# Kernel tuning notes

Hardware: AMD Instinct MI355X
Metric: run time of the kernel (lower is better)

## Reference

```python
import jax, jax.numpy as jnp
import numpy as np

# Module config (init_kwargs)
CIN, COUT, KH, KW = 256, 256, 3, 3
STRIDE, PADDING = 1, 1
T = 64                 # psum chunk size along the reduction (K) axis
NBITS = 8              # saturating accumulator bits (signed)
QMAX = (1 << (NBITS - 1)) - 1   # 127
QMIN = QMAX - (1 << NBITS) + 1  # -128


def setup_inputs() -> dict:
    key = jax.random.key(0)
    k1, k2 = jax.random.split(key)
    x = jax.random.normal(k1, (8, CIN, 56, 56), dtype=jnp.float32)
    # nn.Parameter(torch.rand((N,1)) * 0.001)
    weights = jax.random.uniform(k2, (CIN * COUT * KH * KW, 1), dtype=jnp.float32) * 0.001
    return {"x": x, "weights": weights}


def reference(x, weights):
    B, _, H, W = x.shape
    OH = (H - KH + 2 * PADDING) // STRIDE + 1
    OW = (W - KW + 2 * PADDING) // STRIDE + 1

    w = weights.reshape(COUT, CIN, KH, KW)
    # per-output-channel scaling factor, detached
    scale = jax.lax.stop_gradient(jnp.mean(jnp.abs(w), axis=(1, 2, 3), keepdims=True))
    # binarize with STE: sign(w).detach() - clamp(w).detach() + clamp(w)
    wc = jnp.clip(w, -1.0, 1.0)
    wb = jax.lax.stop_gradient(jnp.sign(w) - wc) + wc

    # unfold (im2col); channel varies slowest -> matches torch.nn.functional.unfold
    patches = jax.lax.conv_general_dilated_patches(
        x, (KH, KW), (STRIDE, STRIDE), [(PADDING, PADDING), (PADDING, PADDING)]
    )  # [B, CIN*KH*KW, OH*OW... (spatial)]
    K = CIN * KH * KW
    L = OH * OW
    A = patches.reshape(B, K, L).transpose(0, 2, 1)  # [B, L, K]
    X = wb.reshape(COUT, K).T                        # [K, COUT]

    pad = (-K) % T
    if pad:
        A = jnp.pad(A, ((0, 0), (0, 0), (0, pad)))
        X = jnp.pad(X, ((0, pad), (0, 0)))
    nT = (K + pad) // T

    A4 = A.reshape(B, L, nT, T)        # chunked reduction axis
    X3 = X.reshape(nT, T, COUT)
    # per-chunk partial sums (satmm_cuda.forward_psum)
    psum = jnp.einsum('blnt,ntc->nblc', A4, X3)  # [nT, B, L, COUT]

    # saturating sequential accumulation: reduce(lambda a,b: clip(a+b, QMIN, QMAX))
    def step(carry, p):
        return jnp.clip(carry + p, QMIN, QMAX), None
    y_flat, _ = jax.lax.scan(step, psum[0], psum[1:])  # [B, L, COUT]

    y = y_flat.transpose(0, 2, 1).reshape(B, COUT, OH, OW)
    y = y * scale.reshape(1, -1, 1, 1)
    # psum returned in the original [B, L, COUT, nT] layout
    return y, psum.transpose(1, 2, 3, 0)
```

## Files before the change

kernel.cpp:

```cpp
#include <hip/hip_runtime.h>
#include <hip/hip_bf16.h>

#define CIN 256
#define COUT 256
#define HW 56
#define BATCH 8
#define L_SPATIAL 3136
#define K_TOTAL 2304
#define NT 36
#define NH 18
#define ROWF (COUT * NT)
#define KSTRIDE 2312
#define BUF_BYTES (16 * KSTRIDE * 2)
#define CARRY_OFF (2 * BUF_BYTES)
#define LDS_BYTES (CARRY_OFF + 8192)
#define MT_TOTAL 1568
#define TILES_PER_IMG 196
#define NWG 256
#define QMAXF 127.0f
#define QMINF -128.0f

typedef short bf16x8 __attribute__((ext_vector_type(8)));
typedef float f32x4 __attribute__((ext_vector_type(4)));
typedef float f32x2 __attribute__((ext_vector_type(2)));

__device__ __forceinline__ void nt_store4(float* p, f32x4 v) {
  __builtin_nontemporal_store(v, reinterpret_cast<f32x4*>(p));
}

__device__ __forceinline__ void lgkm_barrier() {
  __builtin_amdgcn_sched_barrier(0);
  asm volatile("s_waitcnt lgkmcnt(0)" ::: "memory");
  __builtin_amdgcn_s_barrier();
  asm volatile("" ::: "memory");
  __builtin_amdgcn_sched_barrier(0);
}

__global__ __launch_bounds__(256) void prep_kernel(
    const float* __restrict__ w, unsigned short* __restrict__ bsign,
    float* __restrict__ scale) {
  const int c = blockIdx.x;
  const int t = threadIdx.x;
  const float* row = w + (size_t)c * K_TOTAL;
  unsigned short* out = bsign + (size_t)c * K_TOTAL;
  float acc = 0.0f;
#pragma unroll
  for (int j = 0; j < 9; ++j) {
    const int k = t + 256 * j;
    const float v = row[k];
    acc += __builtin_fabsf(v);
    out[k] = (v > 0.0f) ? (unsigned short)0x3F80
           : ((v < 0.0f) ? (unsigned short)0xBF80 : (unsigned short)0);
  }
#pragma unroll
  for (int o = 32; o > 0; o >>= 1) acc += __shfl_down(acc, o, 64);
  __shared__ float red[4];
  if ((t & 63) == 0) red[t >> 6] = acc;
  __syncthreads();
  if (t == 0) scale[c] = (red[0] + red[1] + red[2] + red[3]) * (1.0f / 2304.0f);
}

__device__ __forceinline__ void build_atile(
    const float* __restrict__ xb, unsigned short* __restrict__ Atile,
    int tid, int l0) {
  const int ml = tid & 15;
  const int grp = tid >> 4;
  const int l = l0 + ml;
  const int oh = l / HW;
  const int ow = l - oh * HW;
  unsigned short* arow = Atile + ml * KSTRIDE;
  for (int r = grp; r < 768; r += 64) {
    const int ci = r / 3;
    const int kh = r - ci * 3;
    const int hh = oh + kh - 1;
    const bool hv = ((unsigned)hh < (unsigned)HW);
    const float* xr = xb + (ci * HW + hh) * HW;
    const int kb = ci * 9 + kh * 3;
#pragma unroll
    for (int kw = 0; kw < 3; ++kw) {
      const int wv = ow + kw - 1;
      float v = 0.0f;
      if (hv && ((unsigned)wv < (unsigned)HW)) v = xr[wv];
      __hip_bfloat16 bv = __float2bfloat16(v);
      arow[kb + kw] = *reinterpret_cast<unsigned short*>(&bv);
    }
  }
}

template <int H>
__device__ __forceinline__ void compute18(
    const unsigned short* __restrict__ aptr,
    const unsigned short* __restrict__ bptr,
    f32x4* __restrict__ ps, f32x4& sacc) {
  const f32x4 zero = {0.0f, 0.0f, 0.0f, 0.0f};
  const unsigned short* ap = aptr + H * NH * 64;
  const unsigned short* bp = bptr + H * NH * 64;
  bf16x8 b0[3], b1[3];
  b0[0] = *reinterpret_cast<const bf16x8*>(bp);
  b1[0] = *reinterpret_cast<const bf16x8*>(bp + 32);
  b0[1] = *reinterpret_cast<const bf16x8*>(bp + 64);
  b1[1] = *reinterpret_cast<const bf16x8*>(bp + 96);
#pragma unroll
  for (int j = 0; j < NH; ++j) {
    if (j + 2 < NH) {
      b0[(j + 2) % 3] = *reinterpret_cast<const bf16x8*>(bp + (j + 2) * 64);
      b1[(j + 2) % 3] = *reinterpret_cast<const bf16x8*>(bp + (j + 2) * 64 + 32);
    }
    bf16x8 a0 = *reinterpret_cast<const bf16x8*>(ap + j * 64);
    bf16x8 a1 = *reinterpret_cast<const bf16x8*>(ap + j * 64 + 32);
    f32x4 acc = __builtin_amdgcn_mfma_f32_16x16x32_bf16(a0, b0[j % 3], zero, 0, 0, 0);
    acc = __builtin_amdgcn_mfma_f32_16x16x32_bf16(a1, b1[j % 3], acc, 0, 0, 0);
    ps[j] = acc;
    if (H == 0) {
      if (j == 0) {
        sacc = acc;
      } else {
#pragma unroll
        for (int e = 0; e < 4; ++e)
          sacc[e] = __builtin_amdgcn_fmed3f(sacc[e] + acc[e], QMINF, QMAXF);
      }
    }
  }
}

__global__ __launch_bounds__(1024, 4) void satconv_kernel(
    const float* __restrict__ x, const unsigned short* __restrict__ bsign,
    const float* __restrict__ scale, float* __restrict__ y_out,
    float* __restrict__ psum_out) {
  extern __shared__ char smem[];
  float* carryb = (float*)(smem + CARRY_OFF);

  const int tid = threadIdx.x;
  const int w = blockIdx.x;
  const int b_img = w & 7;
  const float* xb = x + (size_t)b_img * (CIN * L_SPATIAL);

  const int lane = tid & 63;
  const int cl = lane & 15;
  const int q = lane >> 4;
  const int wave = tid >> 6;
  const int cs = wave >> 1;
  const int h = wave & 1;

  const float sc_s0 = scale[cs * 16 + cl];
  const float sc_s1 = scale[128 + cs * 16 + cl];

  int rel_it[9];
  {
#pragma unroll
    for (int it = 0; it < 9; ++it) {
      const int f = it * 256 + lane * 4;
      const int qq = f / 576;
      const int rem = f - qq * 576;
      const int ci = rem / 36;
      const int n0 = rem - ci * 36;
      rel_it[it] = ((qq << 2) * COUT + ci) * NT + n0;
    }
  }

  int p = 0;
  int t = w;
  build_atile(xb, (unsigned short*)smem, tid, (t >> 3) << 4);
  __syncthreads();

  while (t < MT_TOTAL) {
    const int l0 = (t >> 3) << 4;
    const int m0 = (b_img * TILES_PER_IMG + (t >> 3)) << 4;
    const int mbase = m0 * ROWF;
    unsigned short* Atile = (unsigned short*)(smem + p * BUF_BYTES);
    float* stage = (float*)(smem + (p ^ 1) * BUF_BYTES);
    float* reg = stage + cs * 2304;
    const unsigned short* aptr = Atile + cl * KSTRIDE + q * 8;

    for (int s = 0; s < 2; ++s) {
      const int csub0 = (s << 7) + (cs << 4);
      const int c = csub0 + cl;
      const unsigned short* bptr = bsign + (size_t)c * K_TOTAL + q * 8;

      f32x4 ps[NH];
      f32x4 sacc = {0.0f, 0.0f, 0.0f, 0.0f};
      if (h == 0) compute18<0>(aptr, bptr, ps, sacc);
      else        compute18<1>(aptr, bptr, ps, sacc);

      if (h == 0)
        *reinterpret_cast<f32x4*>(carryb + cs * 256 + lane * 4) = sacc;
      lgkm_barrier();
      if (h == 1) {
        f32x4 cin = *reinterpret_cast<const f32x4*>(carryb + cs * 256 + lane * 4);
#pragma unroll
        for (int j = 0; j < NH; ++j) {
#pragma unroll
          for (int e = 0; e < 4; ++e)
            cin[e] = __builtin_amdgcn_fmed3f(cin[e] + ps[j][e], QMINF, QMAXF);
        }
        const float sc = (s == 0) ? sc_s0 : sc_s1;
        f32x4 yv;
#pragma unroll
        for (int e = 0; e < 4; ++e) yv[e] = cin[e] * sc;
        nt_store4(y_out + ((size_t)b_img * COUT + c) * L_SPATIAL + l0 + (q << 2), yv);
      }

      const int soff = csub0 * NT;
#pragma unroll
      for (int rg = 0; rg < 4; ++rg) {
        {
          float* wr = reg + q * 576 + cl * 36 + h * NH;
          if (h == 0) {
            f32x4 v;
#pragma unroll
            for (int g = 0; g < 4; ++g) {
              v[0] = ps[4 * g + 0][rg]; v[1] = ps[4 * g + 1][rg];
              v[2] = ps[4 * g + 2][rg]; v[3] = ps[4 * g + 3][rg];
              *reinterpret_cast<f32x4*>(wr + 4 * g) = v;
            }
            f32x2 tl = {ps[16][rg], ps[17][rg]};
            *reinterpret_cast<f32x2*>(wr + 16) = tl;
          } else {
            f32x2 tl = {ps[0][rg], ps[1][rg]};
            *reinterpret_cast<f32x2*>(wr) = tl;
            f32x4 v;
#pragma unroll
            for (int g = 0; g < 4; ++g) {
              v[0] = ps[4 * g + 2][rg]; v[1] = ps[4 * g + 3][rg];
              v[2] = ps[4 * g + 4][rg]; v[3] = ps[4 * g + 5][rg];
              *reinterpret_cast<f32x4*>(wr + 2 + 4 * g) = v;
            }
          }
        }
        lgkm_barrier();
        {
          const int rgoff = rg * ROWF + soff;
          const int it0 = (h == 0) ? 0 : 5;
          const int it1 = (h == 0) ? 5 : 9;
          for (int it = it0; it < it1; ++it) {
            f32x4 v = *reinterpret_cast<const f32x4*>(reg + it * 256 + lane * 4);
            nt_store4(psum_out + (size_t)(mbase + rel_it[it] + rgoff), v);
          }
        }
        lgkm_barrier();
      }
    }

    const int tn = t + NWG;
    if (tn < MT_TOTAL)
      build_atile(xb, (unsigned short*)(smem + (p ^ 1) * BUF_BYTES), tid,
                  (tn >> 3) << 4);
    lgkm_barrier();
    p ^= 1;
    t = tn;
  }
}

extern "C" void kernel_launch(void* const* d_in, const int* in_sizes, int n_in,
                              void* d_out, int out_size, void* d_ws, size_t ws_size,
                              hipStream_t stream) {
  const float* x = (const float*)d_in[0];
  const float* w = (const float*)d_in[1];
  float* y = (float*)d_out;
  float* psum = y + (size_t)BATCH * COUT * L_SPATIAL;
  unsigned short* bsign = (unsigned short*)d_ws;
  float* scale = (float*)((char*)d_ws + (size_t)COUT * K_TOTAL * 2);

  prep_kernel<<<COUT, 256, 0, stream>>>(w, bsign, scale);

  hipFuncSetAttribute(reinterpret_cast<const void*>(satconv_kernel),
                      hipFuncAttributeMaxDynamicSharedMemorySize, LDS_BYTES);
  satconv_kernel<<<NWG, 1024, LDS_BYTES, stream>>>(
      x, bsign, scale, y, psum);
}
```

Baseline: 1.229 ms.

## Warp-specialize producer and drainer waves to overlap MFMA compute with psum stores

```diff
diff --git a/kernel.cpp b/kernel.cpp
--- a/kernel.cpp
+++ b/kernel.cpp
@@ -8,12 +8,15 @@
 #define L_SPATIAL 3136
 #define K_TOTAL 2304
 #define NT 36
-#define NH 18
+#define NTH 12
 #define ROWF (COUT * NT)
 #define KSTRIDE 2312
-#define BUF_BYTES (16 * KSTRIDE * 2)
-#define CARRY_OFF (2 * BUF_BYTES)
-#define LDS_BYTES (CARRY_OFF + 8192)
+#define ATILE_BYTES (16 * KSTRIDE * 2)
+#define SLOT0_OFF ATILE_BYTES
+#define SLOT1_OFF (ATILE_BYTES + 36864)
+#define CARRY_OFF (ATILE_BYTES + 73728)
+#define YSTAGE_OFF (CARRY_OFF + 4096)
+#define LDS_BYTES (YSTAGE_OFF + 4096)
 #define MT_TOTAL 1568
 #define TILES_PER_IMG 196
 #define NWG 256
@@ -22,7 +25,6 @@
 
 typedef short bf16x8 __attribute__((ext_vector_type(8)));
 typedef float f32x4 __attribute__((ext_vector_type(4)));
-typedef float f32x2 __attribute__((ext_vector_type(2)));
 
 __device__ __forceinline__ void nt_store4(float* p, f32x4 v) {
   __builtin_nontemporal_store(v, reinterpret_cast<f32x4*>(p));
@@ -62,14 +64,14 @@
 
 __device__ __forceinline__ void build_atile(
     const float* __restrict__ xb, unsigned short* __restrict__ Atile,
-    int tid, int l0) {
+    int tid, int grpN, int l0) {
   const int ml = tid & 15;
   const int grp = tid >> 4;
   const int l = l0 + ml;
   const int oh = l / HW;
   const int ow = l - oh * HW;
   unsigned short* arow = Atile + ml * KSTRIDE;
-  for (int r = grp; r < 768; r += 64) {
+  for (int r = grp; r < 768; r += grpN) {
     const int ci = r / 3;
     const int kh = r - ci * 3;
     const int hh = oh + kh - 1;
@@ -88,21 +90,21 @@
 }
 
 template <int H>
-__device__ __forceinline__ void compute18(
+__device__ __forceinline__ void compute12(
     const unsigned short* __restrict__ aptr,
     const unsigned short* __restrict__ bptr,
     f32x4* __restrict__ ps, f32x4& sacc) {
   const f32x4 zero = {0.0f, 0.0f, 0.0f, 0.0f};
-  const unsigned short* ap = aptr + H * NH * 64;
-  const unsigned short* bp = bptr + H * NH * 64;
+  const unsigned short* ap = aptr + H * NTH * 64;
+  const unsigned short* bp = bptr + H * NTH * 64;
   bf16x8 b0[3], b1[3];
   b0[0] = *reinterpret_cast<const bf16x8*>(bp);
   b1[0] = *reinterpret_cast<const bf16x8*>(bp + 32);
   b0[1] = *reinterpret_cast<const bf16x8*>(bp + 64);
   b1[1] = *reinterpret_cast<const bf16x8*>(bp + 96);
 #pragma unroll
-  for (int j = 0; j < NH; ++j) {
-    if (j + 2 < NH) {
+  for (int j = 0; j < NTH; ++j) {
+    if (j + 2 < NTH) {
       b0[(j + 2) % 3] = *reinterpret_cast<const bf16x8*>(bp + (j + 2) * 64);
       b1[(j + 2) % 3] = *reinterpret_cast<const bf16x8*>(bp + (j + 2) * 64 + 32);
     }
@@ -123,12 +125,35 @@
   }
 }
 
+template <int RG>
+__device__ __forceinline__ void dump_rg(float* slot, int cg, int h, int cl, int q,
+                                        const f32x4* __restrict__ ps) {
+  float* wr = slot + cg * 2304 + q * 576 + cl * 36 + h * NTH;
+#pragma unroll
+  for (int g = 0; g < 3; ++g) {
+    f32x4 v = {ps[4 * g + 0][RG], ps[4 * g + 1][RG],
+               ps[4 * g + 2][RG], ps[4 * g + 3][RG]};
+    *reinterpret_cast<f32x4*>(wr + 4 * g) = v;
+  }
+}
+
+__device__ __forceinline__ void drain_rg(
+    const char* smem, int slotOff, float* __restrict__ psum_out,
+    int addrBase, const int* __restrict__ rel_it, int ci, int lane) {
+  const float* sl = (const float*)(smem + slotOff);
+#pragma unroll
+  for (int it = 0; it < 9; ++it) {
+    f32x4 v = *reinterpret_cast<const f32x4*>(sl + (ci * 9 + it) * 256 + lane * 4);
+    nt_store4(psum_out + (size_t)(addrBase + rel_it[it]), v);
+  }
+}
+
 __global__ __launch_bounds__(1024, 4) void satconv_kernel(
     const float* __restrict__ x, const unsigned short* __restrict__ bsign,
     const float* __restrict__ scale, float* __restrict__ y_out,
     float* __restrict__ psum_out) {
   extern __shared__ char smem[];
-  float* carryb = (float*)(smem + CARRY_OFF);
+  unsigned short* Atile = (unsigned short*)smem;
 
   const int tid = threadIdx.x;
   const int w = blockIdx.x;
@@ -136,118 +161,136 @@
   const float* xb = x + (size_t)b_img * (CIN * L_SPATIAL);
 
   const int lane = tid & 63;
+  const int wave = tid >> 6;
   const int cl = lane & 15;
   const int q = lane >> 4;
-  const int wave = tid >> 6;
-  const int cs = wave >> 1;
-  const int h = wave & 1;
-
-  const float sc_s0 = scale[cs * 16 + cl];
-  const float sc_s1 = scale[128 + cs * 16 + cl];
+  const bool is_prod = (wave < 12);
+  const int cg = wave & 3;
+  const int h = wave >> 2;
+  const int ci = is_prod ? 0 : (wave - 12);
+
+  float scv[4];
+#pragma unroll
+  for (int st = 0; st < 4; ++st)
+    scv[st] = scale[(st >> 1) * 128 + cg * 32 + (st & 1) * 16 + cl];
 
   int rel_it[9];
-  {
-#pragma unroll
-    for (int it = 0; it < 9; ++it) {
-      const int f = it * 256 + lane * 4;
-      const int qq = f / 576;
-      const int rem = f - qq * 576;
-      const int ci = rem / 36;
-      const int n0 = rem - ci * 36;
-      rel_it[it] = ((qq << 2) * COUT + ci) * NT + n0;
-    }
-  }
-
-  int p = 0;
-  int t = w;
-  build_atile(xb, (unsigned short*)smem, tid, (t >> 3) << 4);
+#pragma unroll
+  for (int it = 0; it < 9; ++it) {
+    const int f = (ci * 9 + it) * 256 + lane * 4;
+    const int cg_d = f / 2304;
+    const int r1 = f - cg_d * 2304;
+    const int q_d = r1 / 576;
+    const int r2 = r1 - q_d * 576;
+    const int cl_d = r2 / 36;
+    const int n0 = r2 - cl_d * 36;
+    rel_it[it] = (q_d * 4) * ROWF + (cg_d * 32 + cl_d) * 36 + n0;
+  }
+
+  build_atile(xb, Atile, tid, 64, ((w) >> 3) << 4);
   __syncthreads();
 
-  while (t < MT_TOTAL) {
-    const int l0 = (t >> 3) << 4;
-    const int m0 = (b_img * TILES_PER_IMG + (t >> 3)) << 4;
-    const int mbase = m0 * ROWF;
-    unsigned short* Atile = (unsigned short*)(smem + p * BUF_BYTES);
-    float* stage = (float*)(smem + (p ^ 1) * BUF_BYTES);
-    float* reg = stage + cs * 2304;
-    const unsigned short* aptr = Atile + cl * KSTRIDE + q * 8;
-
-    for (int s = 0; s < 2; ++s) {
-      const int csub0 = (s << 7) + (cs << 4);
-      const int c = csub0 + cl;
-      const unsigned short* bptr = bsign + (size_t)c * K_TOTAL + q * 8;
-
-      f32x4 ps[NH];
+  const unsigned short* aptr = Atile + cl * KSTRIDE + q * 8;
+  float* const slot0 = (float*)(smem + SLOT0_OFF);
+  float* const slot1 = (float*)(smem + SLOT1_OFF);
+  float* const carryb = (float*)(smem + CARRY_OFF);
+  float* const ystage = (float*)(smem + YSTAGE_OFF);
+
+  int pend = 0;
+  int pend_base2 = 0, pend_base3 = 0, pend_s = 0, pend_tt = 0, pend_l0 = 0;
+
+  for (int t = w; t < MT_TOTAL; t += NWG) {
+    const int tileIdx = t >> 3;
+    const int l0 = tileIdx << 4;
+    const int m0 = (b_img * TILES_PER_IMG + tileIdx) << 4;
+    const int m0row = m0 * ROWF;
+
+#pragma unroll 1
+    for (int st = 0; st < 4; ++st) {
+      const int s = st >> 1, tt = st & 1;
+      const int soff = (s * 128 + tt * 16) * NT;
+
+      f32x4 ps[NTH];
       f32x4 sacc = {0.0f, 0.0f, 0.0f, 0.0f};
-      if (h == 0) compute18<0>(aptr, bptr, ps, sacc);
-      else        compute18<1>(aptr, bptr, ps, sacc);
-
-      if (h == 0)
-        *reinterpret_cast<f32x4*>(carryb + cs * 256 + lane * 4) = sacc;
+
+      if (is_prod) {
+        const int c = s * 128 + cg * 32 + tt * 16 + cl;
+        const unsigned short* bptr = bsign + (size_t)c * K_TOTAL + q * 8;
+        if (h == 0)      compute12<0>(aptr, bptr, ps, sacc);
+        else if (h == 1) compute12<1>(aptr, bptr, ps, sacc);
+        else             compute12<2>(aptr, bptr, ps, sacc);
+        if (h == 0)
+          *reinterpret_cast<f32x4*>(carryb + cg * 256 + cl * 16 + q * 4) = sacc;
+      } else if (pend) {
+        drain_rg(smem, SLOT0_OFF, psum_out, pend_base2, rel_it, ci, lane);
+        drain_rg(smem, SLOT1_OFF, psum_out, pend_base3, rel_it, ci, lane);
+        f32x4 v = *reinterpret_cast<const f32x4*>(ystage + ci * 256 + lane * 4);
+        const int c = pend_s * 128 + ci * 32 + pend_tt * 16 + (lane >> 2);
+        nt_store4(y_out + ((size_t)b_img * COUT + c) * L_SPATIAL + pend_l0 +
+                      ((lane & 3) << 2), v);
+      }
       lgkm_barrier();
-      if (h == 1) {
-        f32x4 cin = *reinterpret_cast<const f32x4*>(carryb + cs * 256 + lane * 4);
-#pragma unroll
-        for (int j = 0; j < NH; ++j) {
-#pragma unroll
-          for (int e = 0; e < 4; ++e)
-            cin[e] = __builtin_amdgcn_fmed3f(cin[e] + ps[j][e], QMINF, QMAXF);
+
+      if (is_prod) {
+        dump_rg<0>(slot0, cg, h, cl, q, ps);
+        dump_rg<1>(slot1, cg, h, cl, q, ps);
+        if (h == 1) {
+          f32x4 cin = *reinterpret_cast<const f32x4*>(carryb + cg * 256 + cl * 16 + q * 4);
+#pragma unroll
+          for (int j = 0; j < NTH; ++j)
+#pragma unroll
+            for (int e = 0; e < 4; ++e)
+              cin[e] = __builtin_amdgcn_fmed3f(cin[e] + ps[j][e], QMINF, QMAXF);
+          *reinterpret_cast<f32x4*>(carryb + cg * 256 + cl * 16 + q * 4) = cin;
         }
-        const float sc = (s == 0) ? sc_s0 : sc_s1;
-        f32x4 yv;
-#pragma unroll
-        for (int e = 0; e < 4; ++e) yv[e] = cin[e] * sc;
-        nt_store4(y_out + ((size_t)b_img * COUT + c) * L_SPATIAL + l0 + (q << 2), yv);
-      }
-
-      const int soff = csub0 * NT;
-#pragma unroll
-      for (int rg = 0; rg < 4; ++rg) {
-        {
-          float* wr = reg + q * 576 + cl * 36 + h * NH;
-          if (h == 0) {
-            f32x4 v;
-#pragma unroll
-            for (int g = 0; g < 4; ++g) {
-              v[0] = ps[4 * g + 0][rg]; v[1] = ps[4 * g + 1][rg];
-              v[2] = ps[4 * g + 2][rg]; v[3] = ps[4 * g + 3][rg];
-              *reinterpret_cast<f32x4*>(wr + 4 * g) = v;
-            }
-            f32x2 tl = {ps[16][rg], ps[17][rg]};
-            *reinterpret_cast<f32x2*>(wr + 16) = tl;
-          } else {
-            f32x2 tl = {ps[0][rg], ps[1][rg]};
-            *reinterpret_cast<f32x2*>(wr) = tl;
-            f32x4 v;
-#pragma unroll
-            for (int g = 0; g < 4; ++g) {
-              v[0] = ps[4 * g + 2][rg]; v[1] = ps[4 * g + 3][rg];
-              v[2] = ps[4 * g + 4][rg]; v[3] = ps[4 * g + 5][rg];
-              *reinterpret_cast<f32x4*>(wr + 2 + 4 * g) = v;
-            }
-          }
+      }
+      lgkm_barrier();
+
+      if (is_prod) {
+        if (h == 2) {
+          f32x4 cin = *reinterpret_cast<const f32x4*>(carryb + cg * 256 + cl * 16 + q * 4);
+#pragma unroll
+          for (int j = 0; j < NTH; ++j)
+#pragma unroll
+            for (int e = 0; e < 4; ++e)
+              cin[e] = __builtin_amdgcn_fmed3f(cin[e] + ps[j][e], QMINF, QMAXF);
+          const float sc = scv[st];
+          f32x4 yv;
+#pragma unroll
+          for (int e = 0; e < 4; ++e) yv[e] = cin[e] * sc;
+          *reinterpret_cast<f32x4*>(ystage + cg * 256 + cl * 16 + q * 4) = yv;
         }
-        lgkm_barrier();
-        {
-          const int rgoff = rg * ROWF + soff;
-          const int it0 = (h == 0) ? 0 : 5;
-          const int it1 = (h == 0) ? 5 : 9;
-          for (int it = it0; it < it1; ++it) {
-            f32x4 v = *reinterpret_cast<const f32x4*>(reg + it * 256 + lane * 4);
-            nt_store4(psum_out + (size_t)(mbase + rel_it[it] + rgoff), v);
-          }
-        }
-        lgkm_barrier();
-      }
+      } else {
+        drain_rg(smem, SLOT0_OFF, psum_out, m0row + 0 * ROWF + soff, rel_it, ci, lane);
+        drain_rg(smem, SLOT1_OFF, psum_out, m0row + 1 * ROWF + soff, rel_it, ci, lane);
+      }
+      lgkm_barrier();
+
+      if (is_prod) {
+        dump_rg<2>(slot0, cg, h, cl, q, ps);
+        dump_rg<3>(slot1, cg, h, cl, q, ps);
+      }
+      lgkm_barrier();
+
+      pend = 1;
+      pend_base2 = m0row + 2 * ROWF + soff;
+      pend_base3 = m0row + 3 * ROWF + soff;
+      pend_s = s; pend_tt = tt; pend_l0 = l0;
     }
 
     const int tn = t + NWG;
-    if (tn < MT_TOTAL)
-      build_atile(xb, (unsigned short*)(smem + (p ^ 1) * BUF_BYTES), tid,
-                  (tn >> 3) << 4);
+    if (is_prod) {
+      if (tn < MT_TOTAL) build_atile(xb, Atile, tid, 48, (tn >> 3) << 4);
+    } else if (pend) {
+      drain_rg(smem, SLOT0_OFF, psum_out, pend_base2, rel_it, ci, lane);
+      drain_rg(smem, SLOT1_OFF, psum_out, pend_base3, rel_it, ci, lane);
+      f32x4 v = *reinterpret_cast<const f32x4*>(ystage + ci * 256 + lane * 4);
+      const int c = pend_s * 128 + ci * 32 + pend_tt * 16 + (lane >> 2);
+      nt_store4(y_out + ((size_t)b_img * COUT + c) * L_SPATIAL + pend_l0 +
+                    ((lane & 3) << 2), v);
+    }
+    pend = 0;
     lgkm_barrier();
-    p ^= 1;
-    t = tn;
   }
 }
 
```

Measured after the change: 1.167 ms. -5.0%, faster.
